# Performance work log

Hardware: AMD Instinct MI355X
Metric: run time of the kernel (lower is better)

## Reference

```python
import jax, jax.numpy as jnp
import numpy as np

WS = 7
SHIFT = 3
S_SIZE = 20.0
T_SIZE = 1.0
DIM = 256
HEADS = 8
EPS = 1e-5


def _rel_pos_index(ws):
    coords = np.stack(np.meshgrid(np.arange(ws), np.arange(ws), indexing='ij')).reshape(2, -1)
    rel = (coords[:, :, None] - coords[:, None, :]).transpose(1, 2, 0).copy()
    rel[..., 0] += ws - 1
    rel[..., 1] += ws - 1
    rel[..., 0] *= 2 * ws - 1
    return rel.sum(-1)  # (ws*ws, ws*ws)


def _calc_masks(H, W, ws, shift, s_size, t_size):
    # shifted-window mask (standard Swin)
    img = np.zeros((H, W), dtype=np.float32)
    sl = (slice(0, -ws), slice(-ws, -shift), slice(-shift, None))
    cnt = 0
    for h in sl:
        for w in sl:
            img[h, w] = cnt
            cnt += 1
    N = ws * ws
    mw = img.reshape(H // ws, ws, W // ws, ws).transpose(0, 2, 1, 3).reshape(-1, N)
    am = np.where((mw[:, None, :] - mw[:, :, None]) != 0, -100.0, 0.0).astype(np.float32)
    # physical 'cone' masks
    kmh = 1000.0 / 3600.0
    cv_min, cv_max = 60.0 * kmh, 100.0 * kmh
    cw_min, cw_max = 10.0 * kmh, 25.0 * kmh
    r = np.arange(ws)
    rr, cc = np.meshgrid(r, r, indexing='ij')
    coords = np.stack([rr.ravel(), cc.ravel()], -1)
    delta = coords[:, None, :] - coords[None, :, :]
    dy = delta[..., 0].astype(np.float32) * s_size
    dt = delta[..., 1].astype(np.float32) * t_size
    eye = np.eye(N, dtype=bool)
    dt_pos = dt > 0
    safe_dt = np.where(dt_pos, dt, 1.0)
    sp = np.where(dt_pos, dy / safe_dt, 0.0)
    allow_v = (dt_pos & (dy >= 0) & (sp >= cv_min) & (sp <= cv_max)) | eye
    cone_v = np.where(allow_v, 0.0, -100.0).astype(np.float32)
    spw = np.where(dt_pos, np.abs(dy) / safe_dt, 0.0)
    allow_w = (dt_pos & (dy <= 0) & (spw >= cw_min) & (spw <= cw_max)) | eye
    cone_w = np.where(allow_w, 0.0, -100.0).astype(np.float32)
    return am + cone_v[None], am + cone_w[None]


def _ln(x, g, b):
    mu = jnp.mean(x, -1, keepdims=True)
    var = jnp.mean((x - mu) ** 2, -1, keepdims=True)
    return (x - mu) / jnp.sqrt(var + EPS) * g + b


def _win_part(x, ws):
    B, H, W, C = x.shape
    return x.reshape(B, H // ws, ws, W // ws, ws, C).transpose(0, 1, 3, 2, 4, 5).reshape(-1, ws * ws, C)


def _win_rev(w, ws, H, W):
    B = w.shape[0] // ((H // ws) * (W // ws))
    return w.reshape(B, H // ws, W // ws, ws, ws, -1).transpose(0, 1, 3, 2, 4, 5).reshape(B, H, W, -1)


def _wattn(xw, qkv_w, qkv_b, proj_w, proj_b, rpb, mask, rpi, nH):
    Bw, N, Ch = xw.shape
    hd = Ch // nH
    qkv = (xw @ qkv_w.T + qkv_b).reshape(Bw, N, 3, nH, hd).transpose(2, 0, 3, 1, 4)
    q = qkv[0] * (hd ** -0.5)
    attn = jnp.einsum('bhnd,bhmd->bhnm', q, qkv[1])
    bias = rpb[rpi.reshape(-1)].reshape(N, N, nH).transpose(2, 0, 1)
    attn = attn + bias[None]
    nW = mask.shape[0]
    attn = (attn.reshape(Bw // nW, nW, nH, N, N) + mask[None, :, None]).reshape(Bw, nH, N, N)
    attn = jax.nn.softmax(attn, axis=-1)
    out = jnp.einsum('bhnm,bhmd->bhnd', attn, qkv[2]).transpose(0, 2, 1, 3).reshape(Bw, N, Ch)
    return out @ proj_w.T + proj_b


def _forward(H, W, x, norm1_g, norm1_b, norm2_g, norm2_b,
             qkv_w1, qkv_b1, proj_w1, proj_b1, rpb1,
             qkv_w2, qkv_b2, proj_w2, proj_b2, rpb2,
             fc1_w, fc1_b, fc2_w, fc2_b):
    B, L, C = x.shape
    ws, shift = WS, SHIFT
    m1, m2 = _calc_masks(H, W, ws, shift, S_SIZE, T_SIZE)
    m1, m2 = jnp.asarray(m1), jnp.asarray(m2)
    rpi = jnp.asarray(_rel_pos_index(ws))
    nH = HEADS // 2
    shortcut = x
    xn = _ln(x, norm1_g, norm1_b).reshape(B, H, W, C)
    halves = []
    for xh, qw, qb, pw, pb, rpb, m in (
        (xn[..., :C // 2], qkv_w1, qkv_b1, proj_w1, proj_b1, rpb1, m1),
        (xn[..., C // 2:], qkv_w2, qkv_b2, proj_w2, proj_b2, rpb2, m2),
    ):
        sx = jnp.roll(xh, (-shift, -shift), (1, 2))
        aw = _wattn(_win_part(sx, ws), qw, qb, pw, pb, rpb, m, rpi, nH)
        halves.append(jnp.roll(_win_rev(aw, ws, H, W), (shift, shift), (1, 2)))
    x = shortcut + jnp.concatenate(halves, -1).reshape(B, L, C)
    h = _ln(x, norm2_g, norm2_b)
    h = jax.nn.gelu(h @ fc1_w.T + fc1_b, approximate=False)
    return x + (h @ fc2_w.T + fc2_b)


def setup_inputs() -> dict:
    key = jax.random.key(0)
    B, H, W, C = 2, 224, 224, DIM
    Ch = C // 2
    hid = 4 * C
    nrpb = (2 * WS - 1) * (2 * WS - 1)
    nHh = HEADS // 2
    ks = jax.random.split(key, 16)
    p = lambda k, shape: 0.02 * jax.random.normal(k, shape, dtype=jnp.float32)
    return {
        'x': jax.random.normal(ks[0], (B, H * W, C), dtype=jnp.float32),
        'H': H, 'W': W,
        'norm1_g': jnp.ones((C,), jnp.float32), 'norm1_b': jnp.zeros((C,), jnp.float32),
        'norm2_g': jnp.ones((C,), jnp.float32), 'norm2_b': jnp.zeros((C,), jnp.float32),
        'qkv_w1': p(ks[1], (3 * Ch, Ch)), 'qkv_b1': jnp.zeros((3 * Ch,), jnp.float32),
        'proj_w1': p(ks[2], (Ch, Ch)), 'proj_b1': jnp.zeros((Ch,), jnp.float32),
        'rpb1': p(ks[3], (nrpb, nHh)),
        'qkv_w2': p(ks[4], (3 * Ch, Ch)), 'qkv_b2': jnp.zeros((3 * Ch,), jnp.float32),
        'proj_w2': p(ks[5], (Ch, Ch)), 'proj_b2': jnp.zeros((Ch,), jnp.float32),
        'rpb2': p(ks[6], (nrpb, nHh)),
        'fc1_w': p(ks[7], (hid, C)), 'fc1_b': jnp.zeros((hid,), jnp.float32),
        'fc2_w': p(ks[8], (C, hid)), 'fc2_b': jnp.zeros((C,), jnp.float32),
    }


def reference(x, H, W, norm1_g, norm1_b, norm2_g, norm2_b,
              qkv_w1, qkv_b1, proj_w1, proj_b1, rpb1,
              qkv_w2, qkv_b2, proj_w2, proj_b2, rpb2,
              fc1_w, fc1_b, fc2_w, fc2_b):
    return _forward(H, W, x, norm1_g, norm1_b, norm2_g, norm2_b,
                    qkv_w1, qkv_b1, proj_w1, proj_b1, rpb1,
                    qkv_w2, qkv_b2, proj_w2, proj_b2, rpb2,
                    fc1_w, fc1_b, fc2_w, fc2_b)
```

## Files before the change

### kernel.cpp

```cpp
#include <hip/hip_runtime.h>

using u16 = unsigned short;
typedef short short8 __attribute__((ext_vector_type(8)));
typedef float f32x4 __attribute__((ext_vector_type(4)));

#define T_TOK 100352

__device__ __forceinline__ float bf2f(u16 u) {
    return __uint_as_float(((unsigned int)u) << 16);
}
__device__ __forceinline__ u16 f2bf(float f) {
    unsigned int u = __float_as_uint(f);
    u += 0x7fffu + ((u >> 16) & 1u);
    return (u16)(u >> 16);
}

__device__ __forceinline__ void ld_g2l16(const u16* g, u16* l) {
    __builtin_amdgcn_global_load_lds((const __attribute__((address_space(1))) void*)g,
                                     (__attribute__((address_space(3))) void*)l,
                                     16, 0, 0);
}

__global__ __launch_bounds__(256) void cvt_all_k(const float* __restrict__ q1,
                                                 const float* __restrict__ q2,
                                                 const float* __restrict__ p1,
                                                 const float* __restrict__ p2,
                                                 const float* __restrict__ f1,
                                                 const float* __restrict__ f2,
                                                 u16* __restrict__ dst) {
    int i = blockIdx.x * 256 + threadIdx.x;
    if (i >= 655360) return;
    const float* s; int off;
    if (i < 49152)       { s = q1; off = 0; }
    else if (i < 98304)  { s = q2; off = 49152; }
    else if (i < 114688) { s = p1; off = 98304; }
    else if (i < 131072) { s = p2; off = 114688; }
    else if (i < 393216) { s = f1; off = 131072; }
    else                 { s = f2; off = 393216; }
    dst[i] = f2bf(s[i - off]);
}

__global__ __launch_bounds__(256) void bias_tbl_k(const float* __restrict__ rpb0,
                                                  const float* __restrict__ rpb1,
                                                  float* __restrict__ tbl) {
    int id = blockIdx.x;
    int hsel = id >> 4, wtype = (id >> 2) & 3, h = id & 3;
    const float* rpb = hsel ? rpb1 : rpb0;
    int redge = wtype >> 1, cedge = wtype & 1;
    float* o = tbl + (size_t)id * 2401;
    for (int i = threadIdx.x; i < 2401; i += 256) {
        int n = i / 49, m = i - n * 49;
        int rn = n / 7, cn = n - rn * 7, rm = m / 7, cm = m - rm * 7;
        int rpi = (rn - rm + 6) * 13 + (cn - cm + 6);
        float v = rpb[rpi * 4 + h];
        int grn = redge ? (rn < 4 ? 1 : 2) : 0;
        int grm = redge ? (rm < 4 ? 1 : 2) : 0;
        int gcn = cedge ? (cn < 4 ? 1 : 2) : 0;
        int gcm = cedge ? (cm < 4 ? 1 : 2) : 0;
        if ((grn * 3 + gcn) != (grm * 3 + gcm)) v += -100.0f;
        int dr = rn - rm, dc = cn - cm;
        bool ok;
        if (n == m) ok = true;
        else if (hsel == 0)
            ok = (dc == 1 && dr == 1) || (dc == 2 && dr == 2) ||
                 (dc == 3 && (dr == 3 || dr == 4)) ||
                 (dc == 4 && (dr == 4 || dr == 5)) ||
                 (dc == 5 && (dr == 5 || dr == 6)) ||
                 (dc == 6 && (dr == 5 || dr == 6));
        else
            ok = (dr == -1 && dc >= 3 && dc <= 6) || (dr == -2 && dc == 6);
        if (!ok) v += -100.0f;
        o[i] = v;
    }
}

__global__ __launch_bounds__(256) void ln1_k(const float* __restrict__ x,
                                             const float* __restrict__ g,
                                             const float* __restrict__ b,
                                             u16* __restrict__ xw) {
    int t = blockIdx.x * 4 + (threadIdx.x >> 6);
    int lane = threadIdx.x & 63;
    const float4 v = *(const float4*)(x + (size_t)t * 256 + lane * 4);
    float s = v.x + v.y + v.z + v.w;
    float s2 = v.x * v.x + v.y * v.y + v.z * v.z + v.w * v.w;
#pragma unroll
    for (int off = 1; off < 64; off <<= 1) {
        s += __shfl_xor(s, off);
        s2 += __shfl_xor(s2, off);
    }
    float mean = s * (1.0f / 256.0f);
    float var = s2 * (1.0f / 256.0f) - mean * mean;
    float rstd = 1.0f / sqrtf(var + 1e-5f);

    int bb = (t >= 50176) ? 1 : 0;
    int l = t - bb * 50176;
    int rr = l / 224, cc = l - rr * 224;
    int r2 = rr - 3; if (r2 < 0) r2 += 224;
    int c2 = cc - 3; if (c2 < 0) c2 += 224;
    int wi = r2 / 7, lr = r2 - wi * 7;
    int wj = c2 / 7, lc = c2 - wj * 7;
    size_t mIdx = (size_t)(((bb << 10) + wi * 32 + wj) * 49 + lr * 7 + lc);

    int ch = lane * 4;
    int hsel = ch >> 7, colb = ch & 127;
    const float4 gv = *(const float4*)(g + ch);
    const float4 bv = *(const float4*)(b + ch);
    union { uint2 u; u16 s4[4]; } pk;
    pk.s4[0] = f2bf((v.x - mean) * rstd * gv.x + bv.x);
    pk.s4[1] = f2bf((v.y - mean) * rstd * gv.y + bv.y);
    pk.s4[2] = f2bf((v.z - mean) * rstd * gv.z + bv.z);
    pk.s4[3] = f2bf((v.w - mean) * rstd * gv.w + bv.w);
    *(uint2*)(xw + (size_t)hsel * T_TOK * 128 + mIdx * 128 + colb) = pk.u;
}

__global__ __launch_bounds__(256) void ln2_k(const float* __restrict__ x,
                                             const float* __restrict__ g,
                                             const float* __restrict__ b,
                                             u16* __restrict__ h) {
    int t = blockIdx.x * 4 + (threadIdx.x >> 6);
    int lane = threadIdx.x & 63;
    const float4 v = *(const float4*)(x + (size_t)t * 256 + lane * 4);
    float s = v.x + v.y + v.z + v.w;
    float s2 = v.x * v.x + v.y * v.y + v.z * v.z + v.w * v.w;
#pragma unroll
    for (int off = 1; off < 64; off <<= 1) {
        s += __shfl_xor(s, off);
        s2 += __shfl_xor(s2, off);
    }
    float mean = s * (1.0f / 256.0f);
    float var = s2 * (1.0f / 256.0f) - mean * mean;
    float rstd = 1.0f / sqrtf(var + 1e-5f);
    int ch = lane * 4;
    const float4 gv = *(const float4*)(g + ch);
    const float4 bv = *(const float4*)(b + ch);
    union { uint2 u; u16 s4[4]; } pk;
    pk.s4[0] = f2bf((v.x - mean) * rstd * gv.x + bv.x);
    pk.s4[1] = f2bf((v.y - mean) * rstd * gv.y + bv.y);
    pk.s4[2] = f2bf((v.z - mean) * rstd * gv.z + bv.z);
    pk.s4[3] = f2bf((v.w - mean) * rstd * gv.w + bv.w);
    *(uint2*)(h + (size_t)t * 256 + ch) = pk.u;
}

template <int EPI, int NBN>
__global__ __launch_bounds__(256) void gemm_k(const u16* __restrict__ A0,
                                              const u16* __restrict__ A1,
                                              const u16* __restrict__ W0,
                                              const u16* __restrict__ W1,
                                              const float* __restrict__ b0,
                                              const float* __restrict__ b1,
                                              const float* __restrict__ resid,
                                              void* __restrict__ outp,
                                              int K) {
    __shared__ u16 As[2][128][64];
    __shared__ u16 Bs[2][128][64];
    const int tid = threadIdx.x;
    const int lane = tid & 63;
    const int wave = tid >> 6;
    const int wr = wave >> 1, wc = wave & 1;
    const int id = blockIdx.x;
    const int v = (id & 7) * (gridDim.x >> 3) + (id >> 3);
    const int bm = v / NBN, bn = v - bm * NBN;
    const int hsel = blockIdx.z;
    const u16* A = hsel ? A1 : A0;
    const u16* W = hsel ? W1 : W0;
    const float* bias = hsel ? b1 : b0;
    const int r = lane & 15, kg = lane >> 4;
    const int wbase = wave * 64;

    f32x4 acc[4][4] = {};

    auto STAGE = [&](int buf, int kt) {
#pragma unroll
        for (int i = 0; i < 4; ++i) {
            int idx = i * 256 + tid;
            int row = idx >> 3;
            int cb = (idx & 7) ^ (row & 7);
            int ubase = (i * 256 + wbase) * 8;
            ld_g2l16(A + (size_t)(bm * 128 + row) * K + kt + cb * 8,
                     &As[buf][0][0] + ubase);
            ld_g2l16(W + (size_t)(bn * 128 + row) * K + kt + cb * 8,
                     &Bs[buf][0][0] + ubase);
        }
    };

    const int nk = K >> 6;
    STAGE(0, 0);
    __syncthreads();
    int cur = 0;
    for (int t = 0; t < nk; ++t) {
        if (t + 1 < nk) STAGE(cur ^ 1, (t + 1) << 6);
#pragma unroll
        for (int ks = 0; ks < 2; ++ks) {
            short8 fa[4], fb[4];
#pragma unroll
            for (int mf = 0; mf < 4; ++mf) {
                int ra = wr * 64 + mf * 16 + r;
                fa[mf] = *(const short8*)(&As[cur][ra][((ks * 4 + kg) ^ (ra & 7)) * 8]);
            }
#pragma unroll
            for (int nf = 0; nf < 4; ++nf) {
                int rb = wc * 64 + nf * 16 + r;
                fb[nf] = *(const short8*)(&Bs[cur][rb][((ks * 4 + kg) ^ (rb & 7)) * 8]);
            }
#pragma unroll
            for (int mf = 0; mf < 4; ++mf)
#pragma unroll
                for (int nf = 0; nf < 4; ++nf)
                    acc[mf][nf] = __builtin_amdgcn_mfma_f32_16x16x32_bf16(
                        fa[mf], fb[nf], acc[mf][nf], 0, 0, 0);
        }
        __syncthreads();
        cur ^= 1;
    }

#pragma unroll
    for (int mf = 0; mf < 4; ++mf) {
#pragma unroll
        for (int nf = 0; nf < 4; ++nf) {
#pragma unroll
            for (int j = 0; j < 4; ++j) {
                int row = wr * 64 + mf * 16 + kg * 4 + j;
                int col = wc * 64 + nf * 16 + r;
                int gm = bm * 128 + row;
                int gn = bn * 128 + col;
                float vv = acc[mf][nf][j] + bias[gn];
                if (EPI == 0) {
                    if (gn < 128) vv *= 0.17677669529663687f;
                    ((u16*)outp)[(size_t)hsel * T_TOK * 384 + (size_t)gm * 384 + gn] = f2bf(vv);
                } else if (EPI == 1) {
                    int win = gm / 49, n = gm - win * 49;
                    int bb = win >> 10, w = win & 1023, wi = w >> 5, wj = w & 31;
                    int lr = n / 7, lc = n - lr * 7;
                    int R = wi * 7 + lr + 3;  if (R >= 224) R -= 224;
                    int Cc = wj * 7 + lc + 3; if (Cc >= 224) Cc -= 224;
                    size_t o = ((size_t)bb * 50176 + (size_t)R * 224 + Cc) * 256 +
                               hsel * 128 + gn;
                    ((float*)outp)[o] = resid[o] + vv;
                } else if (EPI == 2) {
                    float y = vv * (1.0f + 0.044715f * vv * vv);
                    float t = __expf(-1.59576912f * y);
                    float gl = vv * __builtin_amdgcn_rcpf(1.0f + t);
                    ((u16*)outp)[(size_t)gm * 1024 + gn] = f2bf(gl);
                } else {
                    size_t o = (size_t)gm * 256 + gn;
                    ((float*)outp)[o] = vv + resid[o];
                }
            }
        }
    }
}

__global__ __launch_bounds__(256) void attn_mfma_k(const u16* __restrict__ qkv,
                                                   const float* __restrict__ btbl,
                                                   u16* __restrict__ attnout) {
    __shared__ u16 P_lds[4][64 * 64];
    __shared__ u16 V_t[4][32 * 64];

    int bid = blockIdx.x;
    int hsel = bid >> 11;
    int win = bid & 2047;
    int w = win & 1023;
    int wtype = (((w >> 5) == 31) ? 2 : 0) + (((w & 31) == 31) ? 1 : 0);
    const u16* src = qkv + (size_t)hsel * T_TOK * 384 + (size_t)win * 49 * 384;
    int tid = threadIdx.x;

    for (int c = tid; c < 1024; c += 256) {
        int m = c >> 4;
        int ms = m < 49 ? m : 48;
        int d0 = (c & 15) * 8;
        uint4 u = *(const uint4*)(src + ms * 384 + 256 + d0);
        const u16* us = (const u16*)&u;
        int mc = m >> 3, ml = m & 7;
#pragma unroll
        for (int i = 0; i < 8; ++i) {
            int d = d0 + i;
            int hh = d >> 5, dl = d & 31;
            V_t[hh][dl * 64 + ((mc ^ (dl & 7)) << 3) + ml] = us[i];
        }
    }

    const int h = tid >> 6, l = tid & 63;
    const int lr = l & 15, lg = l >> 4;

    short8 qa[4], kb[4];
#pragma unroll
    for (int t = 0; t < 4; ++t) {
        int n = t * 16 + lr; int ns = n < 49 ? n : 48;
        qa[t] = *(const short8*)(src + ns * 384 + h * 32 + lg * 8);
        kb[t] = *(const short8*)(src + ns * 384 + 128 + h * 32 + lg * 8);
    }
    f32x4 S[4][4] = {};
#pragma unroll
    for (int ni = 0; ni < 4; ++ni)
#pragma unroll
        for (int mi = 0; mi < 4; ++mi)
            S[ni][mi] = __builtin_amdgcn_mfma_f32_16x16x32_bf16(
                qa[ni], kb[mi], S[ni][mi], 0, 0, 0);

    __syncthreads();

    const float* bias = btbl + ((size_t)((hsel * 4 + wtype) * 4 + h)) * 2401;
    float rs[4][4];
#pragma unroll
    for (int ni = 0; ni < 4; ++ni) {
#pragma unroll
        for (int j = 0; j < 4; ++j) {
            int n = ni * 16 + lg * 4 + j;
            int ns = n < 49 ? n : 48;
            float rsum = 0.0f;
#pragma unroll
            for (int mi = 0; mi < 4; ++mi) {
                int m = mi * 16 + lr;
                int msr = m < 49 ? m : 48;
                float bb = bias[ns * 49 + msr];
                bool valid = (n < 49) && (m < 49);
                float p = valid ? __expf(S[ni][mi][j] + bb) : 0.0f;
                rsum += p;
                int mc = m >> 3;
                P_lds[h][n * 64 + ((mc ^ (n & 7)) << 3) + (m & 7)] = f2bf(p);
            }
#pragma unroll
            for (int off = 1; off < 16; off <<= 1)
                rsum += __shfl_xor(rsum, off);
            rs[ni][j] = rsum;
        }
    }

    f32x4 pv[4][2] = {};
#pragma unroll
    for (int ks = 0; ks < 2; ++ks) {
        int mc = ks * 4 + lg;
        short8 pa[4], vb[2];
#pragma unroll
        for (int ni = 0; ni < 4; ++ni) {
            int n = ni * 16 + lr;
            pa[ni] = *(const short8*)(&P_lds[h][n * 64 + ((mc ^ (n & 7)) << 3)]);
        }
#pragma unroll
        for (int di = 0; di < 2; ++di) {
            int d = di * 16 + lr;
            vb[di] = *(const short8*)(&V_t[h][d * 64 + ((mc ^ (d & 7)) << 3)]);
        }
#pragma unroll
        for (int ni = 0; ni < 4; ++ni)
#pragma unroll
            for (int di = 0; di < 2; ++di)
                pv[ni][di] = __builtin_amdgcn_mfma_f32_16x16x32_bf16(
                    pa[ni], vb[di], pv[ni][di], 0, 0, 0);
    }

#pragma unroll
    for (int ni = 0; ni < 4; ++ni) {
#pragma unroll
        for (int j = 0; j < 4; ++j) {
            int n = ni * 16 + lg * 4 + j;
            if (n < 49) {
                float inv = 1.0f / rs[ni][j];
                u16* op = attnout + (size_t)hsel * T_TOK * 128 +
                          (size_t)(win * 49 + n) * 128 + h * 32;
#pragma unroll
                for (int di = 0; di < 2; ++di)
                    op[di * 16 + lr] = f2bf(pv[ni][di][j] * inv);
            }
        }
    }
}

extern "C" void kernel_launch(void* const* d_in, const int* in_sizes, int n_in,
                              void* d_out, int out_size, void* d_ws, size_t ws_size,
                              hipStream_t stream) {
    (void)in_sizes; (void)n_in; (void)out_size; (void)ws_size;
    const float* x      = (const float*)d_in[0];
    const float* n1g    = (const float*)d_in[3];
    const float* n1b    = (const float*)d_in[4];
    const float* n2g    = (const float*)d_in[5];
    const float* n2b    = (const float*)d_in[6];
    const float* qkvw1  = (const float*)d_in[7];
    const float* qkvb1  = (const float*)d_in[8];
    const float* projw1 = (const float*)d_in[9];
    const float* projb1 = (const float*)d_in[10];
    const float* rpb1   = (const float*)d_in[11];
    const float* qkvw2  = (const float*)d_in[12];
    const float* qkvb2  = (const float*)d_in[13];
    const float* projw2 = (const float*)d_in[14];
    const float* projb2 = (const float*)d_in[15];
    const float* rpb2   = (const float*)d_in[16];
    const float* fc1w   = (const float*)d_in[17];
    const float* fc1b   = (const float*)d_in[18];
    const float* fc2w   = (const float*)d_in[19];
    const float* fc2b   = (const float*)d_in[20];
    float* out = (float*)d_out;

    char* ws = (char*)d_ws;
    u16* qkv_buf = (u16*)ws;
    u16* xw      = (u16*)(ws + 154140672LL);
    u16* hidden  = (u16*)ws;
    float* x2    = (float*)(ws + 205520896LL);
    u16* hbuf    = (u16*)(ws + 308281344LL);
    float* btbl  = (float*)(ws + 359661568LL);
    u16* wbf     = (u16*)(ws + 359968896LL);
    u16* qw0 = wbf;
    u16* qw1 = wbf + 49152;
    u16* pw0 = wbf + 98304;
    u16* pw1 = wbf + 114688;
    u16* f1w = wbf + 131072;
    u16* f2w = wbf + 393216;

    cvt_all_k<<<2560, 256, 0, stream>>>(qkvw1, qkvw2, projw1, projw2, fc1w, fc2w, wbf);
    bias_tbl_k<<<32, 256, 0, stream>>>(rpb1, rpb2, btbl);

    ln1_k<<<25088, 256, 0, stream>>>(x, n1g, n1b, xw);

    gemm_k<0, 3><<<dim3(2352, 1, 2), 256, 0, stream>>>(
        xw, xw + (size_t)T_TOK * 128, qw0, qw1, qkvb1, qkvb2, nullptr, qkv_buf, 128);

    attn_mfma_k<<<4096, 256, 0, stream>>>(qkv_buf, btbl, xw);

    gemm_k<1, 1><<<dim3(784, 1, 2), 256, 0, stream>>>(
        xw, xw + (size_t)T_TOK * 128, pw0, pw1, projb1, projb2, x, x2, 128);

    ln2_k<<<25088, 256, 0, stream>>>(x2, n2g, n2b, hbuf);
    gemm_k<2, 8><<<dim3(6272, 1, 1), 256, 0, stream>>>(
        hbuf, hbuf, f1w, f1w, fc1b, fc1b, nullptr, hidden, 256);
    gemm_k<3, 2><<<dim3(1568, 1, 1), 256, 0, stream>>>(
        hidden, hidden, f2w, f2w, fc2b, fc2b, x2, out, 1024);
}
```

Measured before the change: 683.0 us.

## Use 256x256-tile 512-thread GEMM kernel for MLP fc1/fc2 layers

Adds a new GEMM kernel with 256x256 output tiles, 8 waves per block and a grid swizzle that groups blocks, and uses it for the fc1 (GELU) and fc2 (residual) MLP GEMMs in place of the 128x128 kernel. Larger tiles give more operand reuse per LDS load and fewer global re-reads of A and W. The cost is higher register pressure from 32 accumulators per thread and 128KB of LDS per block, which may limit occupancy. The fc2 grid has only 392 blocks, which may fill the CUs poorly.

New measurement: 673.5 us. About the same (-1.4%).

```diff
diff --git a/kernel.cpp b/kernel.cpp
--- a/kernel.cpp
+++ b/kernel.cpp
@@ -227,7 +227,7 @@
                 if (EPI == 0) {
                     if (gn < 128) vv *= 0.17677669529663687f;
                     ((u16*)outp)[(size_t)hsel * T_TOK * 384 + (size_t)gm * 384 + gn] = f2bf(vv);
-                } else if (EPI == 1) {
+                } else {
                     int win = gm / 49, n = gm - win * 49;
                     int bb = win >> 10, w = win & 1023, wi = w >> 5, wj = w & 31;
                     int lr = n / 7, lc = n - lr * 7;
@@ -236,7 +236,87 @@
                     size_t o = ((size_t)bb * 50176 + (size_t)R * 224 + Cc) * 256 +
                                hsel * 128 + gn;
                     ((float*)outp)[o] = resid[o] + vv;
-                } else if (EPI == 2) {
+                }
+            }
+        }
+    }
+}
+
+template <int EPI, int NBN>
+__global__ __launch_bounds__(512, 2) void gemm256_k(const u16* __restrict__ A,
+                                                    const u16* __restrict__ W,
+                                                    const float* __restrict__ bias,
+                                                    const float* __restrict__ resid,
+                                                    void* __restrict__ outp,
+                                                    int K) {
+    __shared__ u16 As[2][256][64];
+    __shared__ u16 Bs[2][256][64];
+    const int tid = threadIdx.x;
+    const int lane = tid & 63;
+    const int wave = tid >> 6;
+    const int wr = wave >> 2, wc = wave & 3;
+    const int id = blockIdx.x;
+    const int v = (id & 7) * (gridDim.x >> 3) + (id >> 3);
+    const int bm = v / NBN, bn = v - bm * NBN;
+    const int r = lane & 15, kg = lane >> 4;
+    const int wbase = wave * 64;
+
+    f32x4 acc[8][4] = {};
+
+    auto STAGE = [&](int buf, int kt) {
+#pragma unroll
+        for (int i = 0; i < 4; ++i) {
+            int idx = i * 512 + tid;
+            int row = idx >> 3;
+            int cb = (idx & 7) ^ (row & 7);
+            int ubase = (i * 512 + wbase) * 8;
+            ld_g2l16(A + (size_t)(bm * 256 + row) * K + kt + cb * 8,
+                     &As[buf][0][0] + ubase);
+            ld_g2l16(W + (size_t)(bn * 256 + row) * K + kt + cb * 8,
+                     &Bs[buf][0][0] + ubase);
+        }
+    };
+
+    const int nk = K >> 6;
+    STAGE(0, 0);
+    __syncthreads();
+    int cur = 0;
+    for (int t = 0; t < nk; ++t) {
+        if (t + 1 < nk) STAGE(cur ^ 1, (t + 1) << 6);
+#pragma unroll
+        for (int ks = 0; ks < 2; ++ks) {
+            short8 fa[8], fb[4];
+#pragma unroll
+            for (int mf = 0; mf < 8; ++mf) {
+                int ra = wr * 128 + mf * 16 + r;
+                fa[mf] = *(const short8*)(&As[cur][ra][((ks * 4 + kg) ^ (ra & 7)) * 8]);
+            }
+#pragma unroll
+            for (int nf = 0; nf < 4; ++nf) {
+                int rb = wc * 64 + nf * 16 + r;
+                fb[nf] = *(const short8*)(&Bs[cur][rb][((ks * 4 + kg) ^ (rb & 7)) * 8]);
+            }
+#pragma unroll
+            for (int mf = 0; mf < 8; ++mf)
+#pragma unroll
+                for (int nf = 0; nf < 4; ++nf)
+                    acc[mf][nf] = __builtin_amdgcn_mfma_f32_16x16x32_bf16(
+                        fa[mf], fb[nf], acc[mf][nf], 0, 0, 0);
+        }
+        __syncthreads();
+        cur ^= 1;
+    }
+
+#pragma unroll
+    for (int mf = 0; mf < 8; ++mf) {
+#pragma unroll
+        for (int nf = 0; nf < 4; ++nf) {
+#pragma unroll
+            for (int j = 0; j < 4; ++j) {
+                int gm = bm * 256 + wr * 128 + mf * 16 + kg * 4 + j;
+                int gn = bn * 256 + wc * 64 + nf * 16 + r;
+                float vv = acc[mf][nf][j] + bias[gn];
+                if (EPI == 2) {
                     float y = vv * (1.0f + 0.044715f * vv * vv);
                     float t = __expf(-1.59576912f * y);
                     float gl = vv * __builtin_amdgcn_rcpf(1.0f + t);
@@ -420,8 +500,6 @@
         xw, xw + (size_t)T_TOK * 128, pw0, pw1, projb1, projb2, x, x2, 128);
 
     ln2_k<<<25088, 256, 0, stream>>>(x2, n2g, n2b, hbuf);
-    gemm_k<2, 8><<<dim3(6272, 1, 1), 256, 0, stream>>>(
-        hbuf, hbuf, f1w, f1w, fc1b, fc1b, nullptr, hidden, 256);
-    gemm_k<3, 2><<<dim3(1568, 1, 1), 256, 0, stream>>>(
-        hidden, hidden, f2w, f2w, fc2b, fc2b, x2, out, 1024);
-}
+    gemm256_k<2, 4><<<1568, 512, 0, stream>>>(hbuf, f1w, fc1b, nullptr, hidden, 256);
+    gemm256_k<3, 1><<<392, 512, 0, stream>>>(hidden, f2w, fc2b, x2, out, 1024);
+}
```
